# Optimization experiments

Measured on AMD Instinct MI355X. Metric: run time of the kernel, lower is better.

The kernel has to match this reference:

```python
import jax, jax.numpy as jnp
import numpy as np

_R, _C = 64, 64
_N = _R * _C
_SEC_PER_A = 31556926.0
_K = 0.01        # sheet_conductivity
_ALPHA = 1.25    # sheet_flow_exp
_HR = 0.1        # bedrock_step_height
_LR = 2.0        # cavity_spacing
_A = 5e-25       # cavity_closure_coeff
_NEXP = 3        # Glen exponent


def _build_grid():
    idx = np.arange(_N).reshape(_R, _C)
    tail = np.concatenate([idx[:, :-1].ravel(), idx[:-1, :].ravel()]).astype(np.int32)
    head = np.concatenate([idx[:, 1:].ravel(), idx[1:, :].ravel()]).astype(np.int32)
    L = tail.size
    links_at_node = -np.ones((_N, 4), np.int32)
    adj = -np.ones((_N, 4), np.int32)
    cnt = np.zeros(_N, np.int32)
    for l in range(L):
        for a, b in ((tail[l], head[l]), (head[l], tail[l])):
            links_at_node[a, cnt[a]] = l
            adj[a, cnt[a]] = b
            cnt[a] += 1
    r, c = np.divmod(np.arange(_N), _C)
    status = ((r == 0) | (r == _R - 1) | (c == 0) | (c == _C - 1)).astype(np.int32)
    return tail, head, links_at_node, adj, status


def setup_inputs():
    key = jax.random.key(0)
    k = jax.random.split(key, 8)
    tail, head, links_at_node, adj, status = _build_grid()
    L = tail.size
    bedrock = jax.random.uniform(k[0], (_N,), jnp.float32, 0.0, 500.0)
    ice_thk = jax.random.uniform(k[1], (_N,), jnp.float32, 100.0, 1000.0)
    overburden = 917.0 * 9.81 * ice_thk
    base_potential = 1000.0 * 9.81 * bedrock + overburden
    potential = base_potential - 0.3 * overburden + 1e3 * jax.random.normal(k[2], (_N,), jnp.float32)
    sheet_thickness = jax.random.uniform(k[3], (_N,), jnp.float32, 0.01, 0.1)
    sliding_velocity = jax.random.uniform(k[4], (L,), jnp.float32, 10.0, 100.0)
    specific_melt_rate = jax.random.uniform(k[5], (_N,), jnp.float32, 1e-7, 1e-6)
    link_length = jnp.full((L,), 100.0, jnp.float32)
    adj_j = jnp.asarray(adj)
    # mean over ALL 4 slots, padded entries contribute 0 (matches original jnp.mean)
    adj_pot = jnp.mean(jnp.where(adj_j != -1, base_potential[adj_j], 0.0), axis=1)
    inflow = jnp.where(base_potential > adj_pot, 1, -1) * (jnp.asarray(status) > 0)
    return dict(
        base_potential=base_potential,
        overburden_pressure=overburden,
        specific_melt_rate=specific_melt_rate,
        sheet_thickness=sheet_thickness,
        potential=potential,
        sliding_velocity=sliding_velocity,
        link_length=link_length,
        link_tail=jnp.asarray(tail),
        link_head=jnp.asarray(head),
        links_at_node=jnp.asarray(links_at_node),
        inflow_outflow=inflow.astype(jnp.int32),
        dt=3600,
    )


def reference(base_potential, overburden_pressure, specific_melt_rate, sheet_thickness,
              potential, sliding_velocity, link_length, link_tail, link_head,
              links_at_node, inflow_outflow, dt):
    N = base_potential.shape[0]
    t, h = link_tail, link_head
    # --- elliptic operator assembly (per-link, scatter into dense [N,N]) ---
    sheets = 0.5 * (sheet_thickness[t] + sheet_thickness[h])
    inv_grad = jnp.abs((potential[t] - potential[h]) / link_length) ** (-0.5)
    c = -_K * sheets ** _ALPHA * link_length * inv_grad  # symmetric link coefficient (<0)
    dir_row = inflow_outflow == 1  # Dirichlet rows
    ct = jnp.where(dir_row[t], 0.0, c)  # contribution into row tail
    ch = jnp.where(dir_row[h], 0.0, c)  # contribution into row head
    M = (jnp.zeros((N, N), base_potential.dtype)
         .at[t, h].add(ct).at[h, t].add(ch)
         .at[t, t].add(-ct).at[h, h].add(-ch))
    M = jnp.where(dir_row[:, None], jnp.eye(N, dtype=M.dtype), M)
    forcing = jnp.where(dir_row, base_potential - overburden_pressure, specific_melt_rate)
    new_potential = jnp.linalg.solve(M, forcing)
    # --- sheet thickness: map_mean_of_links_to_node then Newton on node-local ODE ---
    valid = links_at_node != -1
    lv = (sliding_velocity / _SEC_PER_A)[links_at_node]  # [N,4]
    sliding = jnp.abs(jnp.sum(jnp.where(valid, lv, 0.0), axis=1)
                      / jnp.maximum(valid.sum(axis=1), 1))
    pressure = base_potential - new_potential
    dtf = jnp.asarray(dt, base_potential.dtype)
    # residual r(h) = h - h0 - dt*(sliding*(HR-h)/LR - A*P^n*h) is LINEAR in h,
    # so Newton converges in one exact step -> closed form:
    new_h = (sheet_thickness + dtf * sliding * _HR / _LR) / (
        1.0 + dtf * (sliding / _LR + _A * pressure ** _NEXP))
    return new_potential, new_h
```

## Files before the change

### kernel.cpp

```cpp
#include <hip/hip_runtime.h>
#include <math.h>


#define NT    512
#define NPT   8
#define NN    4096
#define NC    1024
#define NCC   256
#define CCIT  20
#define MAXIT 40

enum : int { RSHL1 = 0x101, RSHR1 = 0x111,
             ROR8 = 0x128, ROR12 = 0x12C, ROR14 = 0x12E, ROR15 = 0x12F,
             WSHL1 = 0x130, WSHR1 = 0x138 };

template<int CTRL>
__device__ __forceinline__ float dppf(float x) {
    return __int_as_float(__builtin_amdgcn_update_dpp(
        __float_as_int(x), __float_as_int(x), CTRL, 0xF, 0xF, false));
}
template<int CTRL>
__device__ __forceinline__ double dppd(double x) {
    const int lo = __double2loint(x), hi = __double2hiint(x);
    const int l2 = __builtin_amdgcn_update_dpp(lo, lo, CTRL, 0xF, 0xF, false);
    const int h2 = __builtin_amdgcn_update_dpp(hi, hi, CTRL, 0xF, 0xF, false);
    return __hiloint2double(h2, l2);
}
__device__ __forceinline__ void pl16sw(int& a, int& b) {
    asm volatile("s_nop 1\n\tv_permlane16_swap_b32 %0, %1" : "+v"(a), "+v"(b));
}
__device__ __forceinline__ void pl32sw(int& a, int& b) {
    asm volatile("s_nop 1\n\tv_permlane32_swap_b32 %0, %1" : "+v"(a), "+v"(b));
}
__device__ __forceinline__ float shift_dn16(float x, bool inR2) {
    int a = __float_as_int(x), b = __float_as_int(x);
    pl16sw(a, b);
    int g = b, g2 = b;
    pl32sw(g, g2);
    return __int_as_float(inR2 ? g : a);
}
__device__ __forceinline__ float shift_up16(float x, bool inR1) {
    int a = __float_as_int(x), b = __float_as_int(x);
    pl16sw(a, b);
    int d1 = __float_as_int(x), d2 = __float_as_int(x);
    pl32sw(d1, d2);
    int e1 = d2, e2 = d2;
    pl16sw(e1, e2);
    return __int_as_float(inR1 ? e1 : b);
}
__device__ __forceinline__ double dsw32(double x) {
    int lo = __double2loint(x), hi = __double2hiint(x);
    int a = lo, b = lo; pl32sw(a, b);
    int c = hi, d = hi; pl32sw(c, d);
    return __hiloint2double(d, b);
}
__device__ __forceinline__ double dsw16(double x) {
    int lo = __double2loint(x), hi = __double2hiint(x);
    int a = lo, b = lo; pl16sw(a, b);
    int c = hi, d = hi; pl16sw(c, d);
    return __hiloint2double(d, b);
}

__global__ __launch_bounds__(NT, 1)
void sds_solver(const float* __restrict__ base_pot,
                const float* __restrict__ ovb,
                const float* __restrict__ melt,
                const float* __restrict__ sheet,
                const float* __restrict__ pot,
                const float* __restrict__ svel,
                const float* __restrict__ llen,
                const int*   __restrict__ ltail,
                const int*   __restrict__ lhead,
                const int*   __restrict__ lan,
                const int*   __restrict__ inflow,
                const int*   __restrict__ dt_raw,
                float* __restrict__ out,
                int N, int L)
{
    __shared__ __align__(16) float cW[NN], cE[NN], cN[NN], cS[NN];
    __shared__ __align__(16) float FD[NN];
    __shared__ __align__(16) float BNDA[8*128], BNDB[8*128];
    __shared__ __align__(16) float CB[32 + NC + 32];
    __shared__ __align__(16) float CB2[32 + NC + 32];
    __shared__ __align__(16) float EB[32 + NC + 32];
    __shared__ __align__(16) float IDC[32 + NC + 32];
    __shared__ __align__(16) float ccb[NCC];
    __shared__ __align__(16) float cWc_s[NC], cEc_s[NC], cNc_s[NC], cSc_s[NC], dc_s[NC];
    __shared__ double redp[32], redg[16];

    const int tid  = threadIdx.x;
    const int lane = tid & 63;
    const int wid  = tid >> 6;
    const int nb0  = (wid << 9) + lane;

    if (N != NN || L != 8064) return;

    const int dti = dt_raw[0];
    const float as_f = __int_as_float(dti);
    const double dtf = (as_f > 0.5f && as_f < 1.0e12f) ? (double)as_f : (double)dti;

    const float invthf = 0.8f;
    const float c1f = 0.2195122f, c2f = 0.9756098f;
    const float wA = 1.75f;

    {
        const float4 z4 = make_float4(0.f, 0.f, 0.f, 0.f);
        #pragma unroll
        for (int i = tid; i < NN/4; i += NT) {
            ((float4*)cW)[i] = z4; ((float4*)cE)[i] = z4;
            ((float4*)cN)[i] = z4; ((float4*)cS)[i] = z4;
        }
        if (tid < 32) {
            CB[tid]=0.f;  CB[32+NC+tid]=0.f;
            CB2[tid]=0.f; CB2[32+NC+tid]=0.f;
            EB[tid]=0.f;  EB[32+NC+tid]=0.f;
            IDC[tid]=0.f; IDC[32+NC+tid]=0.f;
        }
    }
    __syncthreads();

    for (int l = tid; l < 8064; l += NT) {
        int t, h;
        if (l < 4032) {
            const int r = l / 63;
            const int c2 = l - r * 63;
            t = (r << 6) + c2; h = t + 1;
        } else {
            t = l - 4032; h = t + 64;
        }
        const float sheets = 0.5f * (sheet[t] + sheet[h]);
        const float len = llen[l];
        const float grad = fabsf((pot[t] - pot[h]) / len);
        const float c = -0.01f * (sheets * sqrtf(sqrtf(sheets))) * len / sqrtf(grad);
        const bool dt_ = (inflow[t] == 1);
        const bool dh_ = (inflow[h] == 1);
        if (l < 4032) { cE[t] = dt_ ? 0.f : c; cW[h] = dh_ ? 0.f : c; }
        else          { cS[t] = dt_ ? 0.f : c; cN[h] = dh_ ? 0.f : c; }
    }
    __syncthreads();

    float cw[NPT], ce[NPT], cn[NPT], cs[NPT], dgf[NPT], invdf[NPT];
    double bb[NPT], gg[NPT], xv[NPT], rv[NPT];
    bool dirf[NPT];
    auto ldco = [&]() {
        #pragma unroll
        for (int k = 0; k < NPT; ++k) {
            const int n = nb0 + (k << 6);
            cw[k] = cW[n]; ce[k] = cE[n]; cn[k] = cN[n]; cs[k] = cS[n];
        }
    };
    ldco();
    double gsum = 0.0, gcnt = 0.0;
    #pragma unroll
    for (int k = 0; k < NPT; ++k) {
        const int n = nb0 + (k << 6);
        const bool dir = (inflow[n] == 1);
        const double g = (double)base_pot[n] - (double)ovb[n];
        const double d = -((double)cw[k] + (double)ce[k] + (double)cn[k] + (double)cs[k]);
        const double dg = (dir || d == 0.0) ? 1.0 : d;
        dgf[k] = (float)dg; invdf[k] = (float)(1.0 / dg);
        bb[k] = dir ? g : (double)melt[n];
        gg[k] = g; dirf[k] = dir;
        if (dir) { gsum += g; gcnt += 1.0; }
    }
    {
        #pragma unroll
        for (int off = 32; off > 0; off >>= 1) {
            gsum += __shfl_down(gsum, off, 64);
            gcnt += __shfl_down(gcnt, off, 64);
        }
        if (lane == 0) { redg[2*wid] = gsum; redg[2*wid+1] = gcnt; }
        __syncthreads();
        gsum = 0.0; gcnt = 0.0;
        #pragma unroll
        for (int w = 0; w < NT/64; ++w) { gsum += redg[2*w]; gcnt += redg[2*w+1]; }
    }
    const double gmean = gsum / (gcnt > 0.0 ? gcnt : 1.0);

    auto stB = [&](float* B, const float* v) {
        *(float2*)&B[(wid << 7) + (lane << 1)] = make_float2(v[0], v[7]);
    };
    float qf[NPT];
    auto spmvC = [&](const float* B, const float* vr) {
        const float nb = B[(((wid + 7) & 7) << 7) + (lane << 1) + 1];
        const float sb = B[(((wid + 1) & 7) << 7) + (lane << 1) + 0];
        #pragma unroll
        for (int k = 0; k < NPT; ++k) {
            const float wv = dppf<WSHR1>(vr[k]);
            const float ev = dppf<WSHL1>(vr[k]);
            const float nv = k ? vr[k-1] : nb;
            const float sv = (k < NPT-1) ? vr[k+1] : sb;
            qf[k] = dgf[k]*vr[k] + cw[k]*wv + ce[k]*ev + cn[k]*nv + cs[k]*sv;
        }
    };

    {
        float x0r[NPT];
        #pragma unroll
        for (int k = 0; k < NPT; ++k) {
            const float x0f = (float)(dirf[k] ? gg[k] : gmean);
            xv[k] = (double)x0f; x0r[k] = x0f;
        }
        stB(BNDA, x0r); __syncthreads();
        spmvC(BNDA, x0r);
        #pragma unroll
        for (int k = 0; k < NPT; ++k)
            rv[k] = dirf[k] ? 0.0 : (bb[k] - (double)qf[k]);
    }
    __syncthreads();

    {
        #pragma unroll
        for (int k = 0; k < NPT; ++k) {
            const int n = nb0 + (k << 6);
            if (lane != 0  && inflow[n-1]  == 1) cW[n] = 0.f;
            if (lane != 63 && inflow[n+1]  == 1) cE[n] = 0.f;
            if (n >= 64        && inflow[n-64] == 1) cN[n] = 0.f;
            if (n < NN-64      && inflow[n+64] == 1) cS[n] = 0.f;
            FD[n] = dirf[k] ? 0.f : dgf[k];
        }
    }
    __syncthreads();
    ldco();

    #pragma unroll
    for (int q = 0; q < 2; ++q) {
        const int I = 2*tid + q;
        const int R = tid >> 4, C = I & 31;
        const int na = 128*R + 2*C, nbq = na+1, nc_ = na+64, nd = na+65;
        cEc_s[I] = cE[nbq] + cE[nd];
        cWc_s[I] = cW[na] + cW[nc_];
        cNc_s[I] = cN[na] + cN[nbq];
        cSc_s[I] = cS[nc_] + cS[nd];
        const float d = FD[na]+FD[nbq]+FD[nc_]+FD[nd]
                      + 2.0f*(cE[na] + cE[nc_] + cS[na] + cS[nbq]);
        dc_s[I] = (d > 0.f) ? d : 1.0f;
    }
    __syncthreads();

    float cwc[2], cec[2], cnc[2], csc[2], dcr[2], invdc[2];
    {
        float2 t;
        t = *(float2*)&cWc_s[2*tid]; cwc[0]=t.x; cwc[1]=t.y;
        t = *(float2*)&cEc_s[2*tid]; cec[0]=t.x; cec[1]=t.y;
        t = *(float2*)&cNc_s[2*tid]; cnc[0]=t.x; cnc[1]=t.y;
        t = *(float2*)&cSc_s[2*tid]; csc[0]=t.x; csc[1]=t.y;
        t = *(float2*)&dc_s[2*tid];  dcr[0]=t.x; dcr[1]=t.y;
        invdc[0] = 1.0f/dcr[0]; invdc[1] = 1.0f/dcr[1];
        *(float2*)&IDC[32 + 2*tid] = make_float2(invdc[0], invdc[1]);
    }
    float cwcc[4], cecc[4], cncc[4], cscc[4], dccr[4], invdcc[4];
    if (tid < 64) {
        #pragma unroll
        for (int j = 0; j < 4; ++j) {
            const int Rc = ((tid >> 4) << 2) + j, Cc = tid & 15;
            const int IA = 64*Rc + 2*Cc, IB = IA+1, IC = IA+32, ID = IA+33;
            cecc[j] = cEc_s[IB] + cEc_s[ID];
            cwcc[j] = cWc_s[IA] + cWc_s[IC];
            cncc[j] = cNc_s[IA] + cNc_s[IB];
            cscc[j] = cSc_s[IC] + cSc_s[ID];
            const float d = dc_s[IA]+dc_s[IB]+dc_s[IC]+dc_s[ID]
                          + 2.0f*(cEc_s[IA] + cEc_s[IC] + cSc_s[IA] + cSc_s[IB]);
            dccr[j] = (d > 0.f) ? d : 1.0f;
            invdcc[j] = 1.0f/dccr[j];
        }
    }
    float c1cc[CCIT+1], c2cc[CCIT+1], invthcc;
    {
        const double a = 8e-3, b2 = 2.0;
        const double th = 0.5*(b2+a), de = 0.5*(b2-a), s1 = th/de;
        double rp = 1.0/s1;
        for (int j = 1; j <= CCIT; ++j) {
            const double rj = 1.0/(2.0*s1 - rp);
            c1cc[j] = (float)(rj*rp);
            c2cc[j] = (float)(2.0*rj/de);
            rp = rj;
        }
        invthcc = (float)(1.0/th);
    }
    auto cspmv = [&](const float* B_, float v0, float v1, float& q0, float& q1) {
        const float2 up = *(const float2*)&B_[2*tid];
        const float2 dn = *(const float2*)&B_[64 + 2*tid];
        const float wv = dppf<WSHR1>(v1);
        const float ev = dppf<WSHL1>(v0);
        q0 = dcr[0]*v0 + cwc[0]*wv + cec[0]*v1 + cnc[0]*up.x + csc[0]*dn.x;
        q1 = dcr[1]*v1 + cwc[1]*v0 + cec[1]*ev + cnc[1]*up.y + csc[1]*dn.y;
    };

    double rho_prev = 0.0, pap = 0.0, tol = 0.0;
    double pv[NPT], sv[NPT], rpv[NPT];
    #pragma unroll
    for (int k = 0; k < NPT; ++k) { pv[k]=0.0; sv[k]=0.0; rpv[k]=0.0; }

    for (int it = 0; it < MAXIT; ++it) {
        float f0[NPT], d0[NPT], d1[NPT], zpre[NPT];
        #pragma unroll
        for (int k = 0; k < NPT; ++k) { f0[k] = (float)rv[k] * invdf[k]; d0[k] = f0[k] * invthf; }
        stB(BNDA, d0); __syncthreads();
        spmvC(BNDA, d0);
        #pragma unroll
        for (int k = 0; k < NPT; ++k) {
            const float f1 = f0[k] - qf[k]*invdf[k];
            d1[k] = c1f*d0[k] + c2f*f1;
            zpre[k] = d0[k] + d1[k];
            f0[k] = f1;
        }
        stB(BNDB, d1); __syncthreads();
        spmvC(BNDB, d1);

        float r1[NPT], t2[NPT];
        #pragma unroll
        for (int k = 0; k < NPT; ++k) {
            const float fres = f0[k] - qf[k]*invdf[k];
            r1[k] = dirf[k] ? 0.f : dgf[k]*fres;
        }
        #pragma unroll
        for (int k = 0; k < NPT; ++k) t2[k] = r1[k] + dppf<WSHL1>(r1[k]);
        if ((lane & 1) == 0) {
            #pragma unroll
            for (int j = 0; j < 4; ++j)
                CB2[32 + ((wid << 2) + j)*32 + (lane >> 1)] = t2[2*j] + t2[2*j+1];
        }
        __syncthreads();

        float rc[2], f0c[2], d0c[2], d1c[2], qc0, qc1;
        {
            const float2 rcl = *(const float2*)&CB2[32 + 2*tid];
            rc[0] = rcl.x; rc[1] = rcl.y;
        }
        #pragma unroll
        for (int q = 0; q < 2; ++q) {
            f0c[q] = rc[q] * invdc[q];
            d0c[q] = f0c[q] * invthf;
        }
        {
            const float2 ru = *(const float2*)&CB2[2*tid];
            const float2 rd = *(const float2*)&CB2[64 + 2*tid];
            const float2 iu = *(const float2*)&IDC[2*tid];
            const float2 id = *(const float2*)&IDC[64 + 2*tid];
            const float wv = dppf<WSHR1>(d0c[1]);
            const float ev = dppf<WSHL1>(d0c[0]);
            qc0 = dcr[0]*d0c[0] + cwc[0]*wv + cec[0]*d0c[1]
                + cnc[0]*((ru.x*iu.x)*invthf) + csc[0]*((rd.x*id.x)*invthf);
            qc1 = dcr[1]*d0c[1] + cwc[1]*d0c[0] + cec[1]*ev
                + cnc[1]*((ru.y*iu.y)*invthf) + csc[1]*((rd.y*id.y)*invthf);
        }
        {
            const float f1a = f0c[0] - qc0*invdc[0];
            const float f1b = f0c[1] - qc1*invdc[1];
            d1c[0] = c1f*d0c[0] + c2f*f1a;
            d1c[1] = c1f*d0c[1] + c2f*f1b;
            f0c[0] = f1a; f0c[1] = f1b;
        }
        *(float2*)&EB[32 + 2*tid] = make_float2(d1c[0], d1c[1]);
        __syncthreads();
        cspmv(EB, d1c[0], d1c[1], qc0, qc1);
        {
            const float fra = f0c[0] - qc0*invdc[0];
            const float frb = f0c[1] - qc1*invdc[1];
            *(float2*)&CB[32 + 2*tid] = make_float2(dcr[0]*fra, dcr[1]*frb);
        }
        __syncthreads();

        if (tid < 64) {
            const int cc_c  = tid & 15;
            const int cc_rb = tid >> 4;
            const bool inR1 = (cc_rb == 1), inR2 = (cc_rb == 2);
            float fr[4], dr[4], zc[4];
            #pragma unroll
            for (int j = 0; j < 4; ++j) {
                const int IA = (((cc_rb << 2) + j) << 6) + (cc_c << 1);
                const float rcc = CB[32+IA] + CB[32+IA+1] + CB[32+IA+32] + CB[32+IA+33];
                fr[j] = rcc * invdcc[j];
                dr[j] = fr[j] * invthcc;
                zc[j] = dr[j];
            }
            for (int s = 1; s <= CCIT; ++s) {
                const float zN = shift_dn16(dr[3], inR2);
                const float zS = shift_up16(dr[0], inR1);
                float qcc[4];
                #pragma unroll
                for (int j = 0; j < 4; ++j) {
                    const float wj = dppf<RSHR1>(dr[j]);
                    const float ej = dppf<RSHL1>(dr[j]);
                    const float nj = j ? dr[j-1] : zN;
                    const float sj = (j < 3) ? dr[j+1] : zS;
                    qcc[j] = dccr[j]*dr[j] + cwcc[j]*wj + cecc[j]*ej
                           + cncc[j]*nj + cscc[j]*sj;
                }
                #pragma unroll
                for (int j = 0; j < 4; ++j) {
                    fr[j] -= qcc[j] * invdcc[j];
                    dr[j]  = c1cc[s]*dr[j] + c2cc[s]*fr[j];
                    zc[j] += dr[j];
                }
            }
            #pragma unroll
            for (int j = 0; j < 4; ++j)
                ccb[(((cc_rb << 2) + j) << 4) + cc_c] = zc[j];
        }
        __syncthreads();

        const float ecv = wA * ccb[16*(tid >> 5) + (tid & 15)];
        float zmc[2] = { d0c[0] + d1c[0] + ecv, d0c[1] + d1c[1] + ecv };
        {
            const float2 ru = *(const float2*)&CB2[2*tid];
            const float2 rd = *(const float2*)&CB2[64 + 2*tid];
            const float2 iu = *(const float2*)&IDC[2*tid];
            const float2 id = *(const float2*)&IDC[64 + 2*tid];
            const float2 du = *(const float2*)&EB[2*tid];
            const float2 dd = *(const float2*)&EB[64 + 2*tid];
            const int R = tid >> 4;
            const int Ru = (R > 0)  ? R - 1 : 0;
            const int Rd = (R < 31) ? R + 1 : 31;
            const float ecu = wA * ccb[(Ru >> 1)*16 + (tid & 15)];
            const float ecd = wA * ccb[(Rd >> 1)*16 + (tid & 15)];
            const float upx = ((ru.x*iu.x)*invthf + du.x) + ecu;
            const float upy = ((ru.y*iu.y)*invthf + du.y) + ecu;
            const float dnx = ((rd.x*id.x)*invthf + dd.x) + ecd;
            const float dny = ((rd.y*id.y)*invthf + dd.y) + ecd;
            const float wv = dppf<WSHR1>(zmc[1]);
            const float ev = dppf<WSHL1>(zmc[0]);
            qc0 = dcr[0]*zmc[0] + cwc[0]*wv + cec[0]*zmc[1] + cnc[0]*upx + csc[0]*dnx;
            qc1 = dcr[1]*zmc[1] + cwc[1]*zmc[0] + cec[1]*ev + cnc[1]*upy + csc[1]*dny;
        }
        float fmc[2] = { (rc[0]-qc0)*invdc[0], (rc[1]-qc1)*invdc[1] };
        float d0p[2] = { fmc[0]*invthf, fmc[1]*invthf };
        *(float2*)&CB[32 + 2*tid] = make_float2(d0p[0], d0p[1]);
        __syncthreads();
        cspmv(CB, d0p[0], d0p[1], qc0, qc1);
        {
            const float f1a = fmc[0] - qc0*invdc[0];
            const float f1b = fmc[1] - qc1*invdc[1];
            const float efa = zmc[0] + c1f*d0p[0] + c2f*f1a + d0p[0];
            const float efb = zmc[1] + c1f*d0p[1] + c2f*f1b + d0p[1];
            *(float2*)&EB[32 + 2*tid] = make_float2(efa, efb);
        }
        __syncthreads();

        float ec[4];
        #pragma unroll
        for (int j = 0; j < 4; ++j)
            ec[j] = EB[32 + ((wid << 2) + j)*32 + (lane >> 1)];
        float zmid[NPT], zf[NPT];
        #pragma unroll
        for (int k = 0; k < NPT; ++k)
            zmid[k] = zpre[k] + (dirf[k] ? 0.f : wA * ec[k >> 1]);
        stB(BNDA, zmid); __syncthreads();
        spmvC(BNDA, zmid);
        float fmid[NPT], d0q[NPT];
        #pragma unroll
        for (int k = 0; k < NPT; ++k) {
            fmid[k] = (float)rv[k]*invdf[k] - qf[k]*invdf[k];
            d0q[k]  = fmid[k] * invthf;
        }
        stB(BNDB, d0q); __syncthreads();
        spmvC(BNDB, d0q);
        #pragma unroll
        for (int k = 0; k < NPT; ++k) {
            const float f1 = fmid[k] - qf[k]*invdf[k];
            zf[k] = zmid[k] + d0q[k] + c1f*d0q[k] + c2f*f1;
        }
        stB(BNDA, zf); __syncthreads();
        spmvC(BNDA, zf);

        double rho_n = 0.0, rzp = 0.0, zw = 0.0, pw = 0.0;
        #pragma unroll
        for (int k = 0; k < NPT; ++k) {
            const double zk = (double)zf[k], wk = (double)qf[k];
            rho_n += rv[k]  * zk;
            rzp   += rpv[k] * zk;
            zw    += zk * wk;
            pw    += pv[k] * wk;
        }
        rho_n += dsw32(rho_n); rzp += dsw32(rzp); zw += dsw32(zw); pw += dsw32(pw);
        rho_n += dsw16(rho_n); rzp += dsw16(rzp); zw += dsw16(zw); pw += dsw16(pw);
        rho_n += dppd<ROR8 >(rho_n); rzp += dppd<ROR8 >(rzp); zw += dppd<ROR8 >(zw); pw += dppd<ROR8 >(pw);
        rho_n += dppd<ROR12>(rho_n); rzp += dppd<ROR12>(rzp); zw += dppd<ROR12>(zw); pw += dppd<ROR12>(pw);
        rho_n += dppd<ROR14>(rho_n); rzp += dppd<ROR14>(rzp); zw += dppd<ROR14>(zw); pw += dppd<ROR14>(pw);
        rho_n += dppd<ROR15>(rho_n); rzp += dppd<ROR15>(rzp); zw += dppd<ROR15>(zw); pw += dppd<ROR15>(pw);
        if (lane == 0) {
            redp[4*wid] = rho_n; redp[4*wid+1] = rzp;
            redp[4*wid+2] = zw;  redp[4*wid+3] = pw;
        }
        __syncthreads();
        rho_n = 0.0; rzp = 0.0; zw = 0.0; pw = 0.0;
        #pragma unroll
        for (int w = 0; w < NT/64; ++w) {
            rho_n += redp[4*w];   rzp += redp[4*w+1];
            zw    += redp[4*w+2]; pw  += redp[4*w+3];
        }

        if (it == 0) {
            tol = rho_n * 1e-3 + 1e-300;
            if (!(rho_n > 0.0)) break;
        } else if (rho_n <= tol || !(rho_n > 0.0)) break;
        const double beta = (it == 0) ? 0.0
                          : fmax(0.0, (rho_n - rzp) / rho_prev);
        pap = zw + beta * (2.0 * pw + beta * pap);
        if (!(pap > 0.0)) break;
        const double alpha = rho_n / pap;
        rho_prev = rho_n;
        #pragma unroll
        for (int k = 0; k < NPT; ++k) {
            rpv[k] = rv[k];
            pv[k] = (double)zf[k] + beta * pv[k];
            sv[k] = (double)qf[k] + beta * sv[k];
            xv[k] += alpha * pv[k];
            rv[k] -= alpha * sv[k];
        }
    }

    #pragma unroll
    for (int k = 0; k < NPT; ++k) {
        const int n = nb0 + (k << 6);
        const int r = (wid << 3) + k, c2 = lane;
        const double x = dirf[k] ? gg[k] : xv[k];

        const int hb = r * 63 + c2;
        float sva = 0.0f; int cnt = 0;
        if (c2 > 0)  { sva += svel[hb - 1];       cnt++; }
        if (c2 < 63) { sva += svel[hb];           cnt++; }
        if (r  > 0)  { sva += svel[4032 + n - 64]; cnt++; }
        if (r  < 63) { sva += svel[4032 + n];      cnt++; }
        const double sliding =
            fabs((double)sva / 31556926.0 / (double)(cnt > 0 ? cnt : 1));
        const double P   = (double)base_pot[n] - x;
        const double num = (double)sheet[n] + dtf * sliding * 0.1 / 2.0;
        const double den = 1.0 + dtf * (sliding / 2.0 + 5e-25 * P * P * P);
        out[n]      = (float)x;
        out[NN + n] = (float)(num / den);
    }
}

extern "C" void kernel_launch(void* const* d_in, const int* in_sizes, int n_in,
                              void* d_out, int out_size, void* d_ws, size_t ws_size,
                              hipStream_t stream) {
    const float* base_pot = (const float*)d_in[0];
    const float* ovb      = (const float*)d_in[1];
    const float* melt     = (const float*)d_in[2];
    const float* sheet    = (const float*)d_in[3];
    const float* pot      = (const float*)d_in[4];
    const float* svel     = (const float*)d_in[5];
    const float* llen     = (const float*)d_in[6];
    const int*   ltail    = (const int*)d_in[7];
    const int*   lhead    = (const int*)d_in[8];
    const int*   lan      = (const int*)d_in[9];
    const int*   inflow   = (const int*)d_in[10];
    const int*   dt_raw   = (const int*)d_in[11];
    float* out = (float*)d_out;
    const int N = in_sizes[0];
    const int L = in_sizes[5];

    hipLaunchKernelGGL(sds_solver, dim3(1), dim3(NT), 0, stream,
                       base_pot, ovb, melt, sheet, pot, svel, llen,
                       ltail, lhead, lan, inflow, dt_raw, out, N, L);
}
```

Baseline: 133.7 us.

## Replicate halo residual state per wave to remove two barriers per CG iteration

```diff
diff --git a/kernel.cpp b/kernel.cpp
--- a/kernel.cpp
+++ b/kernel.cpp
@@ -80,6 +80,10 @@
     __shared__ __align__(16) float cW[NN], cE[NN], cN[NN], cS[NN];
     __shared__ __align__(16) float FD[NN];
     __shared__ __align__(16) float BNDA[8*128], BNDB[8*128];
+    __shared__ __align__(16) float ZPB[8*128];
+    __shared__ __align__(16) float DMB[8*128];
+    __shared__ __align__(16) float QFB[8*128];
+    __shared__ __align__(16) double RVB[8*128];
     __shared__ __align__(16) float CB[32 + NC + 32];
     __shared__ __align__(16) float CB2[32 + NC + 32];
     __shared__ __align__(16) float EB[32 + NC + 32];
@@ -140,7 +144,7 @@
     __syncthreads();
 
     float cw[NPT], ce[NPT], cn[NPT], cs[NPT], dgf[NPT], invdf[NPT];
-    double bb[NPT], gg[NPT], xv[NPT], rv[NPT];
+    double xv[NPT], rv[NPT];
     bool dirf[NPT];
     auto ldco = [&]() {
         #pragma unroll
@@ -150,19 +154,37 @@
         }
     };
     ldco();
+    float invdga = 1.0f, invdgb = 1.0f;
+    if (wid > 0) {
+        const int ng = nb0 - 64;
+        const bool dirg = (inflow[ng] == 1);
+        const double d = -((double)cW[ng] + (double)cE[ng] + (double)cN[ng] + (double)cS[ng]);
+        const double dg = (dirg || d == 0.0) ? 1.0 : d;
+        invdga = (float)(1.0 / dg);
+    }
+    if (wid < 7) {
+        const int ng = nb0 + 512;
+        const bool dirg = (inflow[ng] == 1);
+        const double d = -((double)cW[ng] + (double)cE[ng] + (double)cN[ng] + (double)cS[ng]);
+        const double dg = (dirg || d == 0.0) ? 1.0 : d;
+        invdgb = (float)(1.0 / dg);
+    }
     double gsum = 0.0, gcnt = 0.0;
     #pragma unroll
     for (int k = 0; k < NPT; ++k) {
         const int n = nb0 + (k << 6);
         const bool dir = (inflow[n] == 1);
-        const double g = (double)base_pot[n] - (double)ovb[n];
         const double d = -((double)cw[k] + (double)ce[k] + (double)cn[k] + (double)cs[k]);
         const double dg = (dir || d == 0.0) ? 1.0 : d;
         dgf[k] = (float)dg; invdf[k] = (float)(1.0 / dg);
-        bb[k] = dir ? g : (double)melt[n];
-        gg[k] = g; dirf[k] = dir;
-        if (dir) { gsum += g; gcnt += 1.0; }
-    }
+        dirf[k] = dir;
+        if (dir) {
+            const double g = (double)base_pot[n] - (double)ovb[n];
+            gsum += g; gcnt += 1.0;
+        }
+    }
+    *(float2*)&DMB[(wid << 7) + (lane << 1)] =
+        make_float2(dirf[0] ? 0.f : 1.f, dirf[7] ? 0.f : 1.f);
     {
         #pragma unroll
         for (int off = 32; off > 0; off >>= 1) {
@@ -194,20 +216,29 @@
         }
     };
 
+    double rga, rgb, sga = 0.0, sgb = 0.0;
     {
         float x0r[NPT];
         #pragma unroll
         for (int k = 0; k < NPT; ++k) {
-            const float x0f = (float)(dirf[k] ? gg[k] : gmean);
+            const int n = nb0 + (k << 6);
+            const double gz = (double)base_pot[n] - (double)ovb[n];
+            const float x0f = (float)(dirf[k] ? gz : gmean);
             xv[k] = (double)x0f; x0r[k] = x0f;
         }
         stB(BNDA, x0r); __syncthreads();
         spmvC(BNDA, x0r);
         #pragma unroll
-        for (int k = 0; k < NPT; ++k)
-            rv[k] = dirf[k] ? 0.0 : (bb[k] - (double)qf[k]);
+        for (int k = 0; k < NPT; ++k) {
+            const int n = nb0 + (k << 6);
+            rv[k] = dirf[k] ? 0.0 : ((double)melt[n] - (double)qf[k]);
+        }
+        RVB[(wid << 7) + lane]      = rv[0];
+        RVB[(wid << 7) + 64 + lane] = rv[7];
     }
     __syncthreads();
+    rga = (wid > 0) ? RVB[((wid - 1) << 7) + 64 + lane] : 0.0;
+    rgb = (wid < 7) ? RVB[((wid + 1) << 7) + lane]      : 0.0;
 
     {
         #pragma unroll
@@ -287,17 +318,27 @@
         q1 = dcr[1]*v1 + cwc[1]*v0 + cec[1]*ev + cnc[1]*up.y + csc[1]*dn.y;
     };
 
-    double rho_prev = 0.0, pap = 0.0, tol = 0.0;
-    double pv[NPT], sv[NPT], rpv[NPT];
+    double rho_prev = 0.0, pap = 0.0, tol = 0.0, alpha_prev = 0.0;
+    double pv[NPT], sv[NPT];
     #pragma unroll
-    for (int k = 0; k < NPT; ++k) { pv[k]=0.0; sv[k]=0.0; rpv[k]=0.0; }
+    for (int k = 0; k < NPT; ++k) { pv[k]=0.0; sv[k]=0.0; }
 
     for (int it = 0; it < MAXIT; ++it) {
         float f0[NPT], d0[NPT], d1[NPT], zpre[NPT];
         #pragma unroll
         for (int k = 0; k < NPT; ++k) { f0[k] = (float)rv[k] * invdf[k]; d0[k] = f0[k] * invthf; }
-        stB(BNDA, d0); __syncthreads();
-        spmvC(BNDA, d0);
+        const float f0ga = (float)rga * invdga;
+        const float d0ga = f0ga * invthf;
+        const float f0gb = (float)rgb * invdgb;
+        const float d0gb = f0gb * invthf;
+        #pragma unroll
+        for (int k = 0; k < NPT; ++k) {
+            const float wv = dppf<WSHR1>(d0[k]);
+            const float ev = dppf<WSHL1>(d0[k]);
+            const float nv = k ? d0[k-1] : d0ga;
+            const float sv_ = (k < NPT-1) ? d0[k+1] : d0gb;
+            qf[k] = dgf[k]*d0[k] + cw[k]*wv + ce[k]*ev + cn[k]*nv + cs[k]*sv_;
+        }
         #pragma unroll
         for (int k = 0; k < NPT; ++k) {
             const float f1 = f0[k] - qf[k]*invdf[k];
@@ -321,6 +362,7 @@
             for (int j = 0; j < 4; ++j)
                 CB2[32 + ((wid << 2) + j)*32 + (lane >> 1)] = t2[2*j] + t2[2*j+1];
         }
+        *(float2*)&ZPB[(wid << 7) + (lane << 1)] = make_float2(zpre[0], zpre[7]);
         __syncthreads();
 
         float rc[2], f0c[2], d0c[2], d1c[2], qc0, qc1;
@@ -446,8 +488,24 @@
         #pragma unroll
         for (int k = 0; k < NPT; ++k)
             zmid[k] = zpre[k] + (dirf[k] ? 0.f : wA * ec[k >> 1]);
-        stB(BNDA, zmid); __syncthreads();
-        spmvC(BNDA, zmid);
+        {
+            const float zpnb = ZPB[(((wid + 7) & 7) << 7) + (lane << 1) + 1];
+            const float zpsb = ZPB[(((wid + 1) & 7) << 7) + (lane << 1) + 0];
+            const float dmnb = DMB[(((wid + 7) & 7) << 7) + (lane << 1) + 1];
+            const float dmsb = DMB[(((wid + 1) & 7) << 7) + (lane << 1) + 0];
+            const float ecnb = EB[32 + ((wid > 0) ? (4*wid - 1) : 0)*32 + (lane >> 1)];
+            const float ecsb = EB[32 + ((wid < 7) ? (4*wid + 4) : 31)*32 + (lane >> 1)];
+            const float znb = zpnb + dmnb*(wA*ecnb);
+            const float zsb = zpsb + dmsb*(wA*ecsb);
+            #pragma unroll
+            for (int k = 0; k < NPT; ++k) {
+                const float wv = dppf<WSHR1>(zmid[k]);
+                const float ev = dppf<WSHL1>(zmid[k]);
+                const float nv = k ? zmid[k-1] : znb;
+                const float sv_ = (k < NPT-1) ? zmid[k+1] : zsb;
+                qf[k] = dgf[k]*zmid[k] + cw[k]*wv + ce[k]*ev + cn[k]*nv + cs[k]*sv_;
+            }
+        }
         float fmid[NPT], d0q[NPT];
         #pragma unroll
         for (int k = 0; k < NPT; ++k) {
@@ -464,30 +522,31 @@
         stB(BNDA, zf); __syncthreads();
         spmvC(BNDA, zf);
 
-        double rho_n = 0.0, rzp = 0.0, zw = 0.0, pw = 0.0;
+        double rho_n = 0.0, szv = 0.0, zw = 0.0, pw = 0.0;
         #pragma unroll
         for (int k = 0; k < NPT; ++k) {
             const double zk = (double)zf[k], wk = (double)qf[k];
-            rho_n += rv[k]  * zk;
-            rzp   += rpv[k] * zk;
+            rho_n += rv[k] * zk;
+            szv   += sv[k] * zk;
             zw    += zk * wk;
             pw    += pv[k] * wk;
         }
-        rho_n += dsw32(rho_n); rzp += dsw32(rzp); zw += dsw32(zw); pw += dsw32(pw);
-        rho_n += dsw16(rho_n); rzp += dsw16(rzp); zw += dsw16(zw); pw += dsw16(pw);
-        rho_n += dppd<ROR8 >(rho_n); rzp += dppd<ROR8 >(rzp); zw += dppd<ROR8 >(zw); pw += dppd<ROR8 >(pw);
-        rho_n += dppd<ROR12>(rho_n); rzp += dppd<ROR12>(rzp); zw += dppd<ROR12>(zw); pw += dppd<ROR12>(pw);
-        rho_n += dppd<ROR14>(rho_n); rzp += dppd<ROR14>(rzp); zw += dppd<ROR14>(zw); pw += dppd<ROR14>(pw);
-        rho_n += dppd<ROR15>(rho_n); rzp += dppd<ROR15>(rzp); zw += dppd<ROR15>(zw); pw += dppd<ROR15>(pw);
+        rho_n += dsw32(rho_n); szv += dsw32(szv); zw += dsw32(zw); pw += dsw32(pw);
+        rho_n += dsw16(rho_n); szv += dsw16(szv); zw += dsw16(zw); pw += dsw16(pw);
+        rho_n += dppd<ROR8 >(rho_n); szv += dppd<ROR8 >(szv); zw += dppd<ROR8 >(zw); pw += dppd<ROR8 >(pw);
+        rho_n += dppd<ROR12>(rho_n); szv += dppd<ROR12>(szv); zw += dppd<ROR12>(zw); pw += dppd<ROR12>(pw);
+        rho_n += dppd<ROR14>(rho_n); szv += dppd<ROR14>(szv); zw += dppd<ROR14>(zw); pw += dppd<ROR14>(pw);
+        rho_n += dppd<ROR15>(rho_n); szv += dppd<ROR15>(szv); zw += dppd<ROR15>(zw); pw += dppd<ROR15>(pw);
+        *(float2*)&QFB[(wid << 7) + (lane << 1)] = make_float2(qf[0], qf[7]);
         if (lane == 0) {
-            redp[4*wid] = rho_n; redp[4*wid+1] = rzp;
+            redp[4*wid] = rho_n; redp[4*wid+1] = szv;
             redp[4*wid+2] = zw;  redp[4*wid+3] = pw;
         }
         __syncthreads();
-        rho_n = 0.0; rzp = 0.0; zw = 0.0; pw = 0.0;
+        rho_n = 0.0; szv = 0.0; zw = 0.0; pw = 0.0;
         #pragma unroll
         for (int w = 0; w < NT/64; ++w) {
-            rho_n += redp[4*w];   rzp += redp[4*w+1];
+            rho_n += redp[4*w];   szv += redp[4*w+1];
             zw    += redp[4*w+2]; pw  += redp[4*w+3];
         }
 
@@ -495,27 +554,37 @@
             tol = rho_n * 1e-3 + 1e-300;
             if (!(rho_n > 0.0)) break;
         } else if (rho_n <= tol || !(rho_n > 0.0)) break;
+        const double rzp = rho_n + alpha_prev * szv;
         const double beta = (it == 0) ? 0.0
                           : fmax(0.0, (rho_n - rzp) / rho_prev);
         pap = zw + beta * (2.0 * pw + beta * pap);
         if (!(pap > 0.0)) break;
         const double alpha = rho_n / pap;
         rho_prev = rho_n;
-        #pragma unroll
-        for (int k = 0; k < NPT; ++k) {
-            rpv[k] = rv[k];
+        alpha_prev = alpha;
+        #pragma unroll
+        for (int k = 0; k < NPT; ++k) {
             pv[k] = (double)zf[k] + beta * pv[k];
             sv[k] = (double)qf[k] + beta * sv[k];
             xv[k] += alpha * pv[k];
             rv[k] -= alpha * sv[k];
         }
+        {
+            const float qga = (wid > 0) ? QFB[((wid - 1) << 7) + (lane << 1) + 1] : 0.f;
+            sga = (double)qga + beta * sga;
+            rga -= alpha * sga;
+            const float qgb = (wid < 7) ? QFB[((wid + 1) << 7) + (lane << 1) + 0] : 0.f;
+            sgb = (double)qgb + beta * sgb;
+            rgb -= alpha * sgb;
+        }
     }
 
     #pragma unroll
     for (int k = 0; k < NPT; ++k) {
         const int n = nb0 + (k << 6);
         const int r = (wid << 3) + k, c2 = lane;
-        const double x = dirf[k] ? gg[k] : xv[k];
+        const double gz = (double)base_pot[n] - (double)ovb[n];
+        const double x = dirf[k] ? gz : xv[k];
 
         const int hb = r * 63 + c2;
         float sva = 0.0f; int cnt = 0;
```

Measured after the change: 147.2 us. 10.1% more time.
